# Kernel tuning notes

Hardware: AMD Instinct MI355X
Metric: run time of the kernel (lower is better)

Reference implementation:

```python
import jax, jax.numpy as jnp
import numpy as np

N, C, OUT, E, H = 4096, 256, 256, 131072, 8
DH = C // H
EPS = 1e-5


def layer_norm(h, g, b):
    mu = jnp.mean(h, axis=-1, keepdims=True)
    var = jnp.mean(jnp.square(h - mu), axis=-1, keepdims=True)
    return (h - mu) * jax.lax.rsqrt(var + EPS) * g + b


def setup_inputs() -> dict:
    key = jax.random.key(0)
    ks = jax.random.split(key, 12)
    s = 1.0 / np.sqrt(C)
    return {
        "x": jax.random.normal(ks[0], (N, C), jnp.float32),
        "edge_index": jax.random.randint(ks[1], (2, E), 0, N, jnp.int32),
        "edge_attr": jax.random.normal(ks[2], (E, C), jnp.float32),
        # nn.MultiheadAttention params
        "in_proj_w": jax.random.uniform(ks[3], (3 * C, C), jnp.float32, -s, s),
        "in_proj_b": jnp.zeros((3 * C,), jnp.float32),
        "attn_out_w": jax.random.uniform(ks[4], (C, C), jnp.float32, -s, s),
        "attn_out_b": jnp.zeros((C,), jnp.float32),
        # edge_mlp: Linear(3C -> OUT) + LayerNorm(OUT)
        "edge_w": jax.random.uniform(ks[5], (OUT, 3 * C), jnp.float32, -1 / np.sqrt(3 * C), 1 / np.sqrt(3 * C)),
        "edge_b": jax.random.uniform(ks[6], (OUT,), jnp.float32, -1 / np.sqrt(3 * C), 1 / np.sqrt(3 * C)),
        "ln1_g": jnp.ones((OUT,), jnp.float32),
        "ln1_b": jnp.zeros((OUT,), jnp.float32),
        # output_proj: Linear(C + OUT -> OUT)
        "out_w": jax.random.uniform(ks[7], (OUT, C + OUT), jnp.float32, -1 / np.sqrt(C + OUT), 1 / np.sqrt(C + OUT)),
        "out_b": jax.random.uniform(ks[8], (OUT,), jnp.float32, -1 / np.sqrt(C + OUT), 1 / np.sqrt(C + OUT)),
        "ln2_g": jnp.ones((OUT,), jnp.float32),
        "ln2_b": jnp.zeros((OUT,), jnp.float32),
    }


def reference(x, edge_index, edge_attr, in_proj_w, in_proj_b, attn_out_w, attn_out_b,
              edge_w, edge_b, ln1_g, ln1_b, out_w, out_b, ln2_g, ln2_b):
    num_nodes = x.shape[0]
    # --- dense self-attention over all nodes (seq len = N, batch 1) ---
    qkv = x @ in_proj_w.T + in_proj_b            # [N, 3C]
    q, k, v = jnp.split(qkv, 3, axis=-1)
    q = q.reshape(num_nodes, H, DH).transpose(1, 0, 2)  # [H, N, DH]
    k = k.reshape(num_nodes, H, DH).transpose(1, 0, 2)
    v = v.reshape(num_nodes, H, DH).transpose(1, 0, 2)
    scores = jnp.einsum("hqd,hkd->hqk", q, k) / np.sqrt(DH)
    attn = jax.nn.softmax(scores, axis=-1)       # dropout inactive at eval
    ctx = jnp.einsum("hqk,hkd->hqd", attn, v)    # [H, N, DH]
    ctx = ctx.transpose(1, 0, 2).reshape(num_nodes, C)
    x_attn = ctx @ attn_out_w.T + attn_out_b     # [N, C]
    # --- vectorized edge messages: gather -> MLP -> scatter-add ---
    row, col = edge_index[0], edge_index[1]
    msg_in = jnp.concatenate([x[row], x[col], edge_attr], axis=-1)  # [E, 3C]
    msg = jax.nn.relu(layer_norm(msg_in @ edge_w.T + edge_b, ln1_g, ln1_b))
    node_messages = jax.ops.segment_sum(msg, col, num_segments=num_nodes)  # [N, OUT]
    # --- combine, project, residual, norm ---
    combined = jnp.concatenate([x_attn, node_messages], axis=-1)
    out = combined @ out_w.T + out_b
    out = out + x                                # OUT == C so residual fires
    return layer_norm(out, ln2_g, ln2_b)
```

## Files before the change

kernel.cpp:

```cpp
#include <hip/hip_runtime.h>
#include <hip/hip_bf16.h>
#include <math.h>

typedef __bf16 bf16;
typedef __bf16 bf16x8 __attribute__((ext_vector_type(8)));
typedef __bf16 bf16x4 __attribute__((ext_vector_type(4)));
typedef float f32x4 __attribute__((ext_vector_type(4)));
typedef float f32x16 __attribute__((ext_vector_type(16)));

#define MFMA16(a, b, c) __builtin_amdgcn_mfma_f32_16x16x32_bf16((a), (b), (c), 0, 0, 0)
#define MFMA32(a, b, c) __builtin_amdgcn_mfma_f32_32x32x16_bf16((a), (b), (c), 0, 0, 0)

#define N_NODES 4096
#define C_DIM   256
#define E_EDGES 131072
#define APAD    280
#define TPAD    260

__device__ __forceinline__ float ldf(const void* p, int i, bool f32) {
    return f32 ? ((const float*)p)[i] : (float)((const bf16*)p)[i];
}

__device__ __forceinline__ bf16x8 ld8(const void* base, size_t off, bool f32) {
    if (f32) {
        const float* p = (const float*)base + off;
        float4 a = *(const float4*)p;
        float4 b = *(const float4*)(p + 4);
        bf16x8 r;
        r[0] = (bf16)a.x; r[1] = (bf16)a.y; r[2] = (bf16)a.z; r[3] = (bf16)a.w;
        r[4] = (bf16)b.x; r[5] = (bf16)b.y; r[6] = (bf16)b.z; r[7] = (bf16)b.w;
        return r;
    }
    return *(const bf16x8*)((const bf16*)base + off);
}

__device__ __forceinline__ void ld8f(const void* base, int off, bool f32, float* o) {
    if (f32) {
        float4 a = *(const float4*)((const float*)base + off);
        float4 b = *(const float4*)((const float*)base + off + 4);
        o[0] = a.x; o[1] = a.y; o[2] = a.z; o[3] = a.w;
        o[4] = b.x; o[5] = b.y; o[6] = b.z; o[7] = b.w;
    } else {
        bf16x8 r = *(const bf16x8*)((const bf16*)base + off);
#pragma unroll
        for (int j = 0; j < 8; ++j) o[j] = (float)r[j];
    }
}

__device__ __forceinline__ unsigned cvtpk(float a, float b) {
    unsigned r;
    asm("v_cvt_pk_bf16_f32 %0, %1, %2" : "=v"(r) : "v"(a), "v"(b));
    return r;
}
__device__ __forceinline__ void pl32swap(unsigned &a, unsigned &b) {
    asm volatile("v_permlane32_swap_b32 %0, %1" : "+v"(a), "+v"(b));
}

union PW { unsigned u[4]; bf16x8 v; };

__global__ __launch_bounds__(64) void detect_dtype(const void* x, int* flag)
{
    const bf16* xb = (const bf16*)x;
    int tid = threadIdx.x;
    int bad = 0;
    for (int i = tid; i < 4096; i += 64) {
        float v = fabsf((float)xb[i]);
        if (!(v >= 1e-6f && v <= 100.0f)) bad++;
    }
#pragma unroll
    for (int m = 1; m < 64; m <<= 1) bad += __shfl_xor(bad, m);
    if (tid == 0) *flag = (bad > 400) ? 1 : 0;
}

__global__ __launch_bounds__(256) void convert_inputs(
    const void* s0, const void* s1, const void* s2, const void* s3, const void* s4,
    bf16* dst, const int* flag)
{
    int idx = blockIdx.x * 256 + threadIdx.x;
    const void* src; int local;
    if (idx < 1048576)      { src = s0; local = idx; }
    else if (idx < 1245184) { src = s1; local = idx - 1048576; }
    else if (idx < 1310720) { src = s2; local = idx - 1245184; }
    else if (idx < 1507328) { src = s3; local = idx - 1310720; }
    else                    { src = s4; local = idx - 1507328; }
    if (*flag) dst[idx] = (bf16)(((const float*)src)[local]);
    else ((unsigned short*)dst)[idx] = ((const unsigned short*)src)[local];
}

__global__ __launch_bounds__(256) void edge_hist(
    const int* __restrict__ ecol, int* __restrict__ counts)
{
    int e = blockIdx.x * 256 + threadIdx.x;
    atomicAdd(&counts[ecol[e]], 1);
}

__global__ __launch_bounds__(256) void edge_scan(
    const int* __restrict__ counts, int* __restrict__ offsets,
    int* __restrict__ cursor)
{
    __shared__ int part[256];
    __shared__ int pref[257];
    int t = threadIdx.x;
    int base = t * 16;
    int s = 0;
#pragma unroll
    for (int i = 0; i < 16; ++i) s += counts[base + i];
    part[t] = s;
    __syncthreads();
    if (t == 0) {
        int run = 0;
        for (int i = 0; i < 256; ++i) { pref[i] = run; run += part[i]; }
        pref[256] = run;
    }
    __syncthreads();
    int off = pref[t];
#pragma unroll
    for (int i = 0; i < 16; ++i) {
        offsets[base + i] = off;
        cursor[base + i]  = off;
        off += counts[base + i];
    }
    if (t == 255) offsets[4096] = off;
}

__global__ __launch_bounds__(256) void edge_scatter(
    const int* __restrict__ ecol, int* __restrict__ cursor,
    int* __restrict__ eid)
{
    int e = blockIdx.x * 256 + threadIdx.x;
    int pos = atomicAdd(&cursor[ecol[e]], 1);
    eid[pos] = e;
}

__global__ __launch_bounds__(256) void gemm_bt(
    const bf16* __restrict__ A, int lda,
    const bf16* __restrict__ W, int ldw,
    const void* __restrict__ bias,
    void* __restrict__ Cout, int ldc, int c_f32,
    const bf16* __restrict__ resid, int ldr,
    int K, const int* __restrict__ flag)
{
    const bool f32 = (*flag != 0);
    const int wave = threadIdx.x >> 6;
    const int lane = threadIdx.x & 63;
    const int quad = lane >> 4;
    const int l16  = lane & 15;
    const int m_base = blockIdx.x * 32;
    const int n_base = blockIdx.y * 256 + wave * 64;

    const bf16* a0p = A + (size_t)(m_base + l16) * lda + quad * 8;
    const bf16* a1p = a0p + (size_t)16 * lda;
    const bf16* wp  = W + (size_t)(n_base + l16) * ldw + quad * 8;

    f32x4 acc[2][4] = {};
    for (int k = 0; k < K; k += 32) {
        bf16x8 a0 = *(const bf16x8*)(a0p + k);
        bf16x8 a1 = *(const bf16x8*)(a1p + k);
#pragma unroll
        for (int nt = 0; nt < 4; ++nt) {
            bf16x8 b = *(const bf16x8*)(wp + (size_t)nt * 16 * ldw + k);
            acc[0][nt] = MFMA16(a0, b, acc[0][nt]);
            acc[1][nt] = MFMA16(a1, b, acc[1][nt]);
        }
    }
#pragma unroll
    for (int mt = 0; mt < 2; ++mt) {
#pragma unroll
        for (int nt = 0; nt < 4; ++nt) {
            int col = n_base + nt * 16 + l16;
            float bv = bias ? ldf(bias, col, f32) : 0.0f;
#pragma unroll
            for (int r = 0; r < 4; ++r) {
                int row = m_base + mt * 16 + quad * 4 + r;
                float v = acc[mt][nt][r] + bv;
                if (resid) v += (float)resid[(size_t)row * ldr + col];
                if (c_f32) ((float*)Cout)[(size_t)row * ldc + col] = v;
                else       ((bf16*)Cout)[(size_t)row * ldc + col] = (bf16)v;
            }
        }
    }
}

__global__ __launch_bounds__(256) void transpose_v(
    const bf16* __restrict__ qkv, bf16* __restrict__ vt)
{
    __shared__ bf16 t[32][65];
    const int n0 = blockIdx.x * 64;
    const int c0 = blockIdx.y * 32;
    const int tid = threadIdx.x;
    {
        int cl = tid & 31, nl = tid >> 5;
#pragma unroll
        for (int p = 0; p < 8; ++p) {
            int n = nl + p * 8;
            t[cl][n] = qkv[(size_t)(n0 + n) * 768 + 512 + c0 + cl];
        }
    }
    __syncthreads();
    {
        int nn = tid & 63, cc = tid >> 6;
#pragma unroll
        for (int p = 0; p < 8; ++p) {
            int c = cc + p * 4;
            vt[(size_t)(c0 + c) * 4096 + n0 + nn] = t[c][nn];
        }
    }
}

__global__ __launch_bounds__(256) void attn_kernel(
    const bf16* __restrict__ qkv,
    const bf16* __restrict__ vt,
    bf16* __restrict__ ctx)
{
    __shared__ float oL[4][32][33];
    __shared__ float mS[4][32];
    __shared__ float lS[4][32];
    const int tid  = threadIdx.x;
    const int wave = tid >> 6;
    const int lane = tid & 63;
    const int l32  = lane & 31;
    const int hl   = lane >> 5;
    const int h  = blockIdx.x >> 7;
    const int qt = blockIdx.x & 127;

    const float csc = 1.4426950408889634f * 0.17677669529663687f;

    const bf16* qrow = qkv + (size_t)(qt * 32 + l32) * 768 + h * 32 + hl * 8;
    bf16x8 qf1 = *(const bf16x8*)qrow;
    bf16x8 qf2 = *(const bf16x8*)(qrow + 16);

    const bf16* kbp = qkv + 256 + h * 32 + hl * 8;
    const bf16* vrp = vt + (size_t)(h * 32 + l32) * 4096 + hl * 8;

    float mrun = -INFINITY, msc = -INFINITY, lacc = 0.f;
    f32x16 oacc = {};
    const f32x16 z16 = {};

    const int kbeg = wave * 1024;
    for (int k0 = kbeg; k0 < kbeg + 1024; k0 += 32) {
        const bf16* kp = kbp + (size_t)(k0 + l32) * 768;
        bf16x8 kf1 = *(const bf16x8*)kp;
        bf16x8 kf2 = *(const bf16x8*)(kp + 16);
        bf16x8 vf1 = *(const bf16x8*)(vrp + k0);
        bf16x8 vf2 = *(const bf16x8*)(vrp + k0 + 16);

        f32x16 s = MFMA32(kf1, qf1, z16);
        s = MFMA32(kf2, qf2, s);

        float a0 = fmaxf(fmaxf(s[0], s[1]), fmaxf(s[2], s[3]));
        float a1 = fmaxf(fmaxf(s[4], s[5]), fmaxf(s[6], s[7]));
        float a2 = fmaxf(fmaxf(s[8], s[9]), fmaxf(s[10], s[11]));
        float a3 = fmaxf(fmaxf(s[12], s[13]), fmaxf(s[14], s[15]));
        float tm = fmaxf(fmaxf(a0, a1), fmaxf(a2, a3));
        tm = fmaxf(tm, __shfl_xor(tm, 32));

        if (__any(tm > mrun)) {
            float nm = fmaxf(mrun, tm);
            float nmsc = nm * csc;
            float al = exp2f(msc - nmsc);
            mrun = nm; msc = nmsc;
            lacc *= al;
#pragma unroll
            for (int i = 0; i < 16; ++i) oacc[i] *= al;
        }

        float p[16];
#pragma unroll
        for (int i = 0; i < 16; ++i) {
            p[i] = exp2f(__builtin_fmaf(s[i], csc, -msc));
            lacc += p[i];
        }

        unsigned w0 = cvtpk(p[0], p[1]),  w1 = cvtpk(p[2], p[3]);
        unsigned w2 = cvtpk(p[4], p[5]),  w3 = cvtpk(p[6], p[7]);
        unsigned w4 = cvtpk(p[8], p[9]),  w5 = cvtpk(p[10], p[11]);
        unsigned w6 = cvtpk(p[12], p[13]), w7 = cvtpk(p[14], p[15]);
        pl32swap(w0, w2); pl32swap(w1, w3);
        pl32swap(w4, w6); pl32swap(w5, w7);
        PW f1; f1.u[0] = w0; f1.u[1] = w1; f1.u[2] = w2; f1.u[3] = w3;
        PW f2; f2.u[0] = w4; f2.u[1] = w5; f2.u[2] = w6; f2.u[3] = w7;

        oacc = MFMA32(vf1, f1.v, oacc);
        oacc = MFMA32(vf2, f2.v, oacc);
    }

    lacc += __shfl_xor(lacc, 32);
    if (hl == 0) { mS[wave][l32] = mrun; lS[wave][l32] = lacc; }
#pragma unroll
    for (int i = 0; i < 16; ++i) {
        int d = (i & 3) + 8 * (i >> 2) + 4 * hl;
        oL[wave][l32][d] = oacc[i];
    }
    __syncthreads();
    {
        int q = tid >> 3, d0 = (tid & 7) * 4;
        float m0 = mS[0][q], m1 = mS[1][q], m2 = mS[2][q], m3 = mS[3][q];
        float ms = fmaxf(fmaxf(m0, m1), fmaxf(m2, m3));
        float f0 = exp2f((m0 - ms) * csc), f1 = exp2f((m1 - ms) * csc);
        float f2 = exp2f((m2 - ms) * csc), f3 = exp2f((m3 - ms) * csc);
        float ls = lS[0][q] * f0 + lS[1][q] * f1 + lS[2][q] * f2 + lS[3][q] * f3;
        float inv = 1.0f / ls;
        bf16x4 o4;
#pragma unroll
        for (int i = 0; i < 4; ++i) {
            int d = d0 + i;
            float v = (oL[0][q][d] * f0 + oL[1][q][d] * f1 +
                       oL[2][q][d] * f2 + oL[3][q][d] * f3) * inv;
            o4[i] = (bf16)v;
        }
        *(bf16x4*)(ctx + (size_t)(qt * 32 + q) * 256 + h * 32 + d0) = o4;
    }
}

__global__ __launch_bounds__(256) void edge_msg_v3(
    const int* __restrict__ erow, const int* __restrict__ ecol,
    const void* __restrict__ eattr,
    const bf16* __restrict__ ew,
    const void* __restrict__ eb,
    const void* __restrict__ g1, const void* __restrict__ b1,
    const bf16* __restrict__ U, const bf16* __restrict__ V,
    bf16* __restrict__ msg, const int* __restrict__ flag)
{
    __shared__ char smem[64 * APAD * 2];
    bf16* Asm = (bf16*)smem;
    float (*Trow)[TPAD] = (float(*)[TPAD])smem;

    const bool f32 = (*flag != 0);
    const int tid  = threadIdx.x;
    const int wave = tid >> 6;
    const int lane = tid & 63;
    const int quad = lane >> 4;
    const int l16  = lane & 15;
    const int e_base = blockIdx.x * 64;

    bf16x8 breg[8][4];
#pragma unroll
    for (int k0 = 0; k0 < 8; ++k0)
#pragma unroll
        for (int nt = 0; nt < 4; ++nt)
            breg[k0][nt] = *(const bf16x8*)(ew +
                (size_t)(wave * 64 + nt * 16 + l16) * 768 + 512 + k0 * 32 + quad * 8);

    {
        int row   = tid >> 2;
        int cbase = (tid & 3) * 64;
        bf16* dst = Asm + row * APAD + cbase;
        if (!f32) {
            const bf16* src = (const bf16*)eattr + (size_t)(e_base + row) * 256 + cbase;
#pragma unroll
            for (int j = 0; j < 8; ++j)
                *(bf16x8*)(dst + j * 8) = *(const bf16x8*)(src + j * 8);
        } else {
            const float* src = (const float*)eattr + (size_t)(e_base + row) * 256 + cbase;
#pragma unroll
            for (int j = 0; j < 8; ++j) {
                float4 a = *(const float4*)(src + j * 8);
                float4 b = *(const float4*)(src + j * 8 + 4);
                bf16x8 r;
                r[0] = (bf16)a.x; r[1] = (bf16)a.y; r[2] = (bf16)a.z; r[3] = (bf16)a.w;
                r[4] = (bf16)b.x; r[5] = (bf16)b.y; r[6] = (bf16)b.z; r[7] = (bf16)b.w;
                *(bf16x8*)(dst + j * 8) = r;
            }
        }
    }
    __syncthreads();

    f32x4 acc[4][4] = {};
#pragma unroll
    for (int k0 = 0; k0 < 8; ++k0) {
#pragma unroll
        for (int mt = 0; mt < 4; ++mt) {
            bf16x8 af = *(const bf16x8*)(Asm + (mt * 16 + l16) * APAD + k0 * 32 + quad * 8);
#pragma unroll
            for (int nt = 0; nt < 4; ++nt)
                acc[mt][nt] = MFMA16(af, breg[k0][nt], acc[mt][nt]);
        }
    }

    float ebv[4];
#pragma unroll
    for (int nt = 0; nt < 4; ++nt)
        ebv[nt] = ldf(eb, wave * 64 + nt * 16 + l16, f32);

    for (int p = 0; p < 2; ++p) {
        __syncthreads();
#pragma unroll
        for (int mtl = 0; mtl < 2; ++mtl) {
            int mt = p * 2 + mtl;
#pragma unroll
            for (int nt = 0; nt < 4; ++nt)
#pragma unroll
                for (int r = 0; r < 4; ++r)
                    Trow[mtl * 16 + quad * 4 + r][wave * 64 + nt * 16 + l16] =
                        acc[mt][nt][r] + ebv[nt];
        }
        __syncthreads();
        {
            int row = tid >> 3;
            int seg = tid & 7;
            int e = e_base + p * 32 + row;
            int er = erow[e], ec = ecol[e];
            const float* tr = &Trow[row][seg * 32];
            const bf16* up = U + (size_t)er * 256 + seg * 32;
            const bf16* wp = V + (size_t)ec * 256 + seg * 32;
            float v[32];
            float s = 0.f, q = 0.f;
#pragma unroll
            for (int i = 0; i < 4; ++i) {
                float4 ta = *(const float4*)(tr + i * 8);
                float4 tb = *(const float4*)(tr + i * 8 + 4);
                bf16x8 u8 = *(const bf16x8*)(up + i * 8);
                bf16x8 w8 = *(const bf16x8*)(wp + i * 8);
                float t0 = ta.x + (float)u8[0] + (float)w8[0];
                float t1 = ta.y + (float)u8[1] + (float)w8[1];
                float t2 = ta.z + (float)u8[2] + (float)w8[2];
                float t3 = ta.w + (float)u8[3] + (float)w8[3];
                float t4 = tb.x + (float)u8[4] + (float)w8[4];
                float t5 = tb.y + (float)u8[5] + (float)w8[5];
                float t6 = tb.z + (float)u8[6] + (float)w8[6];
                float t7 = tb.w + (float)u8[7] + (float)w8[7];
                v[i*8+0] = t0; v[i*8+1] = t1; v[i*8+2] = t2; v[i*8+3] = t3;
                v[i*8+4] = t4; v[i*8+5] = t5; v[i*8+6] = t6; v[i*8+7] = t7;
                s += ((t0 + t1) + (t2 + t3)) + ((t4 + t5) + (t6 + t7));
                q = __builtin_fmaf(t0, t0, q); q = __builtin_fmaf(t1, t1, q);
                q = __builtin_fmaf(t2, t2, q); q = __builtin_fmaf(t3, t3, q);
                q = __builtin_fmaf(t4, t4, q); q = __builtin_fmaf(t5, t5, q);
                q = __builtin_fmaf(t6, t6, q); q = __builtin_fmaf(t7, t7, q);
            }
#pragma unroll
            for (int msk = 1; msk < 8; msk <<= 1) {
                s += __shfl_xor(s, msk);
                q += __shfl_xor(q, msk);
            }
            float mean = s * (1.0f / 256.0f);
            float var  = q * (1.0f / 256.0f) - mean * mean;
            float rstd = rsqrtf(var + 1e-5f);
            bf16* op = msg + (size_t)e * 256 + seg * 32;
#pragma unroll
            for (int i = 0; i < 4; ++i) {
                float gv[8], bv[8];
                ld8f(g1, seg * 32 + i * 8, f32, gv);
                ld8f(b1, seg * 32 + i * 8, f32, bv);
                bf16x8 o8;
#pragma unroll
                for (int j = 0; j < 8; ++j)
                    o8[j] = (bf16)fmaxf((v[i*8+j] - mean) * rstd * gv[j] + bv[j], 0.0f);
                *(bf16x8*)(op + i * 8) = o8;
            }
        }
    }
}

__global__ __launch_bounds__(256) void node_gather(
    const bf16* __restrict__ msg,
    const int* __restrict__ offsets, const int* __restrict__ eid,
    bf16* __restrict__ combined)
{
    const int wave = threadIdx.x >> 6, lane = threadIdx.x & 63;
    const int node = blockIdx.x * 4 + wave;
    const int start = offsets[node];
    const int cnt   = offsets[node + 1] - start;
    float a0 = 0.f, a1 = 0.f, a2 = 0.f, a3 = 0.f;
    int i = 0;
    for (; i + 4 <= cnt; i += 4) {
        int e0 = eid[start + i],     e1 = eid[start + i + 1];
        int e2 = eid[start + i + 2], e3 = eid[start + i + 3];
        bf16x4 r0 = *(const bf16x4*)(msg + (size_t)e0 * 256 + lane * 4);
        bf16x4 r1 = *(const bf16x4*)(msg + (size_t)e1 * 256 + lane * 4);
        bf16x4 r2 = *(const bf16x4*)(msg + (size_t)e2 * 256 + lane * 4);
        bf16x4 r3 = *(const bf16x4*)(msg + (size_t)e3 * 256 + lane * 4);
        a0 += (float)r0[0] + (float)r1[0] + (float)r2[0] + (float)r3[0];
        a1 += (float)r0[1] + (float)r1[1] + (float)r2[1] + (float)r3[1];
        a2 += (float)r0[2] + (float)r1[2] + (float)r2[2] + (float)r3[2];
        a3 += (float)r0[3] + (float)r1[3] + (float)r2[3] + (float)r3[3];
    }
    for (; i < cnt; ++i) {
        int e = eid[start + i];
        bf16x4 r = *(const bf16x4*)(msg + (size_t)e * 256 + lane * 4);
        a0 += (float)r[0]; a1 += (float)r[1]; a2 += (float)r[2]; a3 += (float)r[3];
    }
    bf16* cp = combined + (size_t)node * 512 + 256 + lane * 4;
    cp[0] = (bf16)a0; cp[1] = (bf16)a1; cp[2] = (bf16)a2; cp[3] = (bf16)a3;
}

__global__ __launch_bounds__(256) void edge_node(
    const bf16* __restrict__ x,
    const int* __restrict__ erow,
    const void* __restrict__ eattr,
    const bf16* __restrict__ ew,
    const void* __restrict__ eb,
    const void* __restrict__ g1, const void* __restrict__ b1,
    const int* __restrict__ offsets, const int* __restrict__ eid,
    bf16* __restrict__ combined, const int* __restrict__ flag)
{
    __shared__ float part[32][4][2];
    const bool f32 = (*flag != 0);
    const int wave = threadIdx.x >> 6;
    const int lane = threadIdx.x & 63;
    const int quad = lane >> 4;
    const int l16  = lane & 15;
    const int n = blockIdx.x;
    const int start = offsets[n];
    const int cnt   = offsets[n + 1] - start;

    float gv[4], bv[4], ebv[4];
#pragma unroll
    for (int nt = 0; nt < 4; ++nt) {
        int col = wave * 64 + nt * 16 + l16;
        gv[nt]  = ldf(g1, col, f32);
        bv[nt]  = ldf(b1, col, f32);
        ebv[nt] = ldf(eb, col, f32);
    }
    const bf16* wp = ew + (size_t)(wave * 64 + l16) * 768 + quad * 8;
    const bf16* xn = x + (size_t)n * 256 + quad * 8;

    f32x4 acc1[4] = {};
#pragma unroll
    for (int kk = 0; kk < 8; ++kk) {
        bf16x8 a = *(const bf16x8*)(xn + kk * 32);
#pragma unroll
        for (int nt = 0; nt < 4; ++nt) {
            bf16x8 b = *(const bf16x8*)(wp + (size_t)nt * 16 * 768 + 256 + kk * 32);
            acc1[nt] = MFMA16(a, b, acc1[nt]);
        }
    }
    float nacc[4] = {0.f, 0.f, 0.f, 0.f};
    for (int c0 = 0; c0 < cnt; c0 += 32) {
        int i0 = c0 + l16;      i0 = (i0 < cnt) ? i0 : 0;
        int i1 = c0 + 16 + l16; i1 = (i1 < cnt) ? i1 : 0;
        int e0 = eid[start + i0];
        int e1 = eid[start + i1];
        const bf16* xr0 = x + (size_t)erow[e0] * 256 + quad * 8;
        const bf16* xr1 = x + (size_t)erow[e1] * 256 + quad * 8;
        f32x4 acc[2][4];
#pragma unroll
        for (int nt = 0; nt < 4; ++nt) { acc[0][nt] = acc1[nt]; acc[1][nt] = acc1[nt]; }
#pragma unroll
        for (int kk = 0; kk < 8; ++kk) {
            bf16x8 a0 = *(const bf16x8*)(xr0 + kk * 32);
            bf16x8 a1 = *(const bf16x8*)(xr1 + kk * 32);
#pragma unroll
            for (int nt = 0; nt < 4; ++nt) {
                bf16x8 b = *(const bf16x8*)(wp + (size_t)nt * 16 * 768 + kk * 32);
                acc[0][nt] = MFMA16(a0, b, acc[0][nt]);
                acc[1][nt] = MFMA16(a1, b, acc[1][nt]);
            }
        }
#pragma unroll
        for (int kk = 0; kk < 8; ++kk) {
            int koff = quad * 8 + kk * 32;
            bf16x8 a0 = ld8(eattr, (size_t)e0 * 256 + koff, f32);
            bf16x8 a1 = ld8(eattr, (size_t)e1 * 256 + koff, f32);
#pragma unroll
            for (int nt = 0; nt < 4; ++nt) {
                bf16x8 b = *(const bf16x8*)(wp + (size_t)nt * 16 * 768 + 512 + kk * 32);
                acc[0][nt] = MFMA16(a0, b, acc[0][nt]);
                acc[1][nt] = MFMA16(a1, b, acc[1][nt]);
            }
        }
#pragma unroll
        for (int mt = 0; mt < 2; ++mt)
#pragma unroll
            for (int nt = 0; nt < 4; ++nt)
#pragma unroll
                for (int r = 0; r < 4; ++r) acc[mt][nt][r] += ebv[nt];
        float ps[2][4], pq[2][4];
#pragma unroll
        for (int mt = 0; mt < 2; ++mt)
#pragma unroll
            for (int r = 0; r < 4; ++r) {
                float s = 0.f, q = 0.f;
#pragma unroll
                for (int nt = 0; nt < 4; ++nt) {
                    float v = acc[mt][nt][r];
                    s += v; q += v * v;
                }
                ps[mt][r] = s; pq[mt][r] = q;
            }
#pragma unroll
        for (int msk = 1; msk < 16; msk <<= 1)
#pragma unroll
            for (int mt = 0; mt < 2; ++mt)
#pragma unroll
                for (int r = 0; r < 4; ++r) {
                    ps[mt][r] += __shfl_xor(ps[mt][r], msk);
                    pq[mt][r] += __shfl_xor(pq[mt][r], msk);
                }
        if (l16 == 0) {
#pragma unroll
            for (int mt = 0; mt < 2; ++mt)
#pragma unroll
                for (int r = 0; r < 4; ++r) {
                    part[mt * 16 + quad * 4 + r][wave][0] = ps[mt][r];
                    part[mt * 16 + quad * 4 + r][wave][1] = pq[mt][r];
                }
        }
        __syncthreads();
#pragma unroll
        for (int mt = 0; mt < 2; ++mt)
#pragma unroll
            for (int r = 0; r < 4; ++r) {
                int row = mt * 16 + quad * 4 + r;
                float s = part[row][0][0] + part[row][1][0] + part[row][2][0] + part[row][3][0];
                float q = part[row][0][1] + part[row][1][1] + part[row][2][1] + part[row][3][1];
                float mean = s * (1.0f / 256.0f);
                float var  = q * (1.0f / 256.0f) - mean * mean;
                float rstd = rsqrtf(var + 1e-5f);
                if ((c0 + row) < cnt) {
#pragma unroll
                    for (int nt = 0; nt < 4; ++nt) {
                        float val = (acc[mt][nt][r] - mean) * rstd * gv[nt] + bv[nt];
                        nacc[nt] += fmaxf(val, 0.0f);
                    }
                }
            }
        __syncthreads();
    }
#pragma unroll
    for (int nt = 0; nt < 4; ++nt) {
        nacc[nt] += __shfl_xor(nacc[nt], 16);
        nacc[nt] += __shfl_xor(nacc[nt], 32);
    }
    if (quad == 0) {
#pragma unroll
        for (int nt = 0; nt < 4; ++nt)
            combined[(size_t)n * 512 + 256 + wave * 64 + nt * 16 + l16] = (bf16)nacc[nt];
    }
}

__global__ __launch_bounds__(256) void ln_out_kernel(
    const float* __restrict__ pre,
    const void* __restrict__ g, const void* __restrict__ bb,
    void* __restrict__ out, const int* __restrict__ flag)
{
    const bool f32 = (*flag != 0);
    const int wave = threadIdx.x >> 6, lane = threadIdx.x & 63;
    const int row = blockIdx.x * 4 + wave;
    float4 v4 = *(const float4*)(pre + (size_t)row * 256 + lane * 4);
    float v[4] = {v4.x, v4.y, v4.z, v4.w};
    float s  = v[0] + v[1] + v[2] + v[3];
    float sq = v[0]*v[0] + v[1]*v[1] + v[2]*v[2] + v[3]*v[3];
#pragma unroll
    for (int msk = 1; msk < 64; msk <<= 1) {
        s  += __shfl_xor(s, msk);
        sq += __shfl_xor(sq, msk);
    }
    float mean = s * (1.0f / 256.0f);
    float var  = sq * (1.0f / 256.0f) - mean * mean;
    float rstd = rsqrtf(var + 1e-5f);
#pragma unroll
    for (int i = 0; i < 4; ++i) {
        int c = lane * 4 + i;
        float r = (v[i] - mean) * rstd * ldf(g, c, f32) + ldf(bb, c, f32);
        if (f32) ((float*)out)[(size_t)row * 256 + c] = r;
        else     ((bf16*)out)[(size_t)row * 256 + c] = (bf16)r;
    }
}

extern "C" void kernel_launch(void* const* d_in, const int* in_sizes, int n_in,
                              void* d_out, int out_size, void* d_ws, size_t ws_size,
                              hipStream_t stream)
{
    const void* x_raw  = d_in[0];
    const int*  eidx   = (const int*)d_in[1];
    const void* eattr  = d_in[2];
    const void* in_w   = d_in[3];
    const void* in_b   = d_in[4];
    const void* ao_w   = d_in[5];
    const void* ao_b   = d_in[6];
    const void* e_w    = d_in[7];
    const void* e_b    = d_in[8];
    const void* g1     = d_in[9];
    const void* b1     = d_in[10];
    const void* o_w    = d_in[11];
    const void* o_b    = d_in[12];
    const void* g2     = d_in[13];
    const void* b2     = d_in[14];

    char* ws = (char*)d_ws;
    bf16*  qkv      = (bf16*)(ws);
    bf16*  vt       = (bf16*)(ws + 6291456);
    bf16*  ctx      = (bf16*)(ws + 8388608);
    bf16*  combined = (bf16*)(ws + 10485760);
    int*   counts   = (int*)(ws + 14680064);
    int*   offsets  = (int*)(ws + 14696448);
    int*   cursor   = (int*)(ws + 14712848);
    int*   eid      = (int*)(ws + 14729232);
    float* out_pre  = (float*)(ws + 18874368);
    bf16*  U        = (bf16*)(ws + 18874368);
    bf16*  V        = (bf16*)(ws + 20971520);
    bf16*  canon    = (bf16*)(ws + 23068672);
    int*   flag     = (int*)(ws + 26345472);
    bf16*  msg      = (bf16*)(ws + 26345728);

    const size_t WS_NEEDED = 93454592;

    bf16* x_bf   = canon;
    bf16* inw_bf = canon + 1048576;
    bf16* aow_bf = canon + 1245184;
    bf16* ew_bf  = canon + 1310720;
    bf16* ow_bf  = canon + 1507328;

    const int* erow = eidx;
    const int* ecol = eidx + E_EDGES;

    detect_dtype<<<dim3(1), 64, 0, stream>>>(x_raw, flag);
    convert_inputs<<<dim3(6400), 256, 0, stream>>>(x_raw, in_w, ao_w, e_w, o_w,
                                                   canon, flag);
    hipMemsetAsync(counts, 0, 16384, stream);
    edge_hist<<<dim3(E_EDGES / 256), 256, 0, stream>>>(ecol, counts);
    edge_scan<<<dim3(1), 256, 0, stream>>>(counts, offsets, cursor);
    edge_scatter<<<dim3(E_EDGES / 256), 256, 0, stream>>>(ecol, cursor, eid);

    gemm_bt<<<dim3(128, 1), 256, 0, stream>>>(x_bf, 256, ew_bf, 768, nullptr,
                                              U, 256, 0, nullptr, 0, 256, flag);
    gemm_bt<<<dim3(128, 1), 256, 0, stream>>>(x_bf, 256, ew_bf + 256, 768, nullptr,
                                              V, 256, 0, nullptr, 0, 256, flag);

    gemm_bt<<<dim3(128, 3), 256, 0, stream>>>(x_bf, 256, inw_bf, 256, in_b,
                                              qkv, 768, 0, nullptr, 0, 256, flag);
    transpose_v<<<dim3(64, 8), 256, 0, stream>>>(qkv, vt);
    attn_kernel<<<dim3(1024), 256, 0, stream>>>(qkv, vt, ctx);
    gemm_bt<<<dim3(128, 1), 256, 0, stream>>>(ctx, 256, aow_bf, 256, ao_b,
                                              combined, 512, 0, nullptr, 0, 256, flag);
    if (ws_size >= WS_NEEDED) {
        edge_msg_v3<<<dim3(E_EDGES / 64), 256, 0, stream>>>(erow, ecol, eattr,
                                                            ew_bf, e_b, g1, b1,
                                                            U, V, msg, flag);
        node_gather<<<dim3(N_NODES / 4), 256, 0, stream>>>(msg, offsets, eid, combined);
    } else {
        edge_node<<<dim3(N_NODES), 256, 0, stream>>>(x_bf, erow, eattr,
                                                     ew_bf, e_b, g1, b1,
                                                     offsets, eid, combined, flag);
    }
    gemm_bt<<<dim3(128, 1), 256, 0, stream>>>(combined, 512, ow_bf, 512, o_b,
                                              out_pre, 256, 1, x_bf, 256, 512, flag);
    ln_out_kernel<<<dim3(N_NODES / 4), 256, 0, stream>>>(out_pre, g2, b2, d_out, flag);
}
```

Measured before the change: 522.0 us.

## Rewrite edge message kernel register-resident, merge U/V GEMMs, fuse output GEMM with LayerNorm

The edge message kernel now computes the edge_attr projection with A operands loaded straight from global memory into registers, 32 edges per block, and does the bias, U/V gather, LayerNorm and ReLU in the MFMA accumulator layout. Row statistics are reduced with cross-lane shuffles plus a tiny shared array, replacing the large LDS staging and transpose buffers. The two U/V GEMM launches are merged into one grid, and the final projection GEMM is fused with residual add and LayerNorm, removing the fp32 intermediate buffer and one launch. Risks: gathered U/V reads become scalar bf16 loads per element, msg stores are no longer vectorised, and A-tile loads are uncoalesced.

```diff
diff --git a/kernel.cpp b/kernel.cpp
--- a/kernel.cpp
+++ b/kernel.cpp
@@ -14,8 +14,6 @@
 #define N_NODES 4096
 #define C_DIM   256
 #define E_EDGES 131072
-#define APAD    280
-#define TPAD    260
 
 __device__ __forceinline__ float ldf(const void* p, int i, bool f32) {
     return f32 ? ((const float*)p)[i] : (float)((const bf16*)p)[i];
@@ -34,19 +32,6 @@
     return *(const bf16x8*)((const bf16*)base + off);
 }
 
-__device__ __forceinline__ void ld8f(const void* base, int off, bool f32, float* o) {
-    if (f32) {
-        float4 a = *(const float4*)((const float*)base + off);
-        float4 b = *(const float4*)((const float*)base + off + 4);
-        o[0] = a.x; o[1] = a.y; o[2] = a.z; o[3] = a.w;
-        o[4] = b.x; o[5] = b.y; o[6] = b.z; o[7] = b.w;
-    } else {
-        bf16x8 r = *(const bf16x8*)((const bf16*)base + off);
-#pragma unroll
-        for (int j = 0; j < 8; ++j) o[j] = (float)r[j];
-    }
-}
-
 __device__ __forceinline__ unsigned cvtpk(float a, float b) {
     unsigned r;
     asm("v_cvt_pk_bf16_f32 %0, %1, %2" : "=v"(r) : "v"(a), "v"(b));
@@ -179,6 +164,48 @@
             }
         }
     }
+}
+
+__global__ __launch_bounds__(256) void gemm_uv(
+    const bf16* __restrict__ x, const bf16* __restrict__ ew,
+    bf16* __restrict__ U, bf16* __restrict__ V)
+{
+    const int wave = threadIdx.x >> 6;
+    const int lane = threadIdx.x & 63;
+    const int quad = lane >> 4;
+    const int l16  = lane & 15;
+    const int m_base = blockIdx.x * 32;
+    bf16* dst = blockIdx.y ? V : U;
+    const bf16* W = ew + blockIdx.y * 256;
+
+    const bf16* a0p = x + (size_t)(m_base + l16) * 256 + quad * 8;
+    const bf16* a1p = a0p + (size_t)16 * 256;
+    const bf16* wp  = W + (size_t)(wave * 64 + l16) * 768 + quad * 8;
+
+    f32x4 acc[2][4] = {};
+#pragma unroll
+    for (int kk = 0; kk < 8; ++kk) {
+        int k = kk * 32;
+        bf16x8 a0 = *(const bf16x8*)(a0p + k);
+        bf16x8 a1 = *(const bf16x8*)(a1p + k);
+#pragma unroll
+        for (int nt = 0; nt < 4; ++nt) {
+            bf16x8 b = *(const bf16x8*)(wp + (size_t)nt * 16 * 768 + k);
+            acc[0][nt] = MFMA16(a0, b, acc[0][nt]);
+            acc[1][nt] = MFMA16(a1, b, acc[1][nt]);
+        }
+    }
+#pragma unroll
+    for (int mt = 0; mt < 2; ++mt)
+#pragma unroll
+        for (int nt = 0; nt < 4; ++nt) {
+            int col = wave * 64 + nt * 16 + l16;
+#pragma unroll
+            for (int r = 0; r < 4; ++r) {
+                int row = m_base + mt * 16 + quad * 4 + r;
+                dst[(size_t)row * 256 + col] = (bf16)acc[mt][nt][r];
+            }
+        }
 }
 
 __global__ __launch_bounds__(256) void transpose_v(
@@ -312,7 +339,7 @@
     }
 }
 
-__global__ __launch_bounds__(256) void edge_msg_v3(
+__global__ __launch_bounds__(256, 4) void edge_msg_v5(
     const int* __restrict__ erow, const int* __restrict__ ecol,
     const void* __restrict__ eattr,
     const bf16* __restrict__ ew,
@@ -321,134 +348,108 @@
     const bf16* __restrict__ U, const bf16* __restrict__ V,
     bf16* __restrict__ msg, const int* __restrict__ flag)
 {
-    __shared__ char smem[64 * APAD * 2];
-    bf16* Asm = (bf16*)smem;
-    float (*Trow)[TPAD] = (float(*)[TPAD])smem;
-
+    __shared__ float stats[32][4][2];
     const bool f32 = (*flag != 0);
     const int tid  = threadIdx.x;
-    const int wave = tid >> 6;
+    const int colq = tid >> 6;
     const int lane = tid & 63;
     const int quad = lane >> 4;
     const int l16  = lane & 15;
-    const int e_base = blockIdx.x * 64;
-
-    bf16x8 breg[8][4];
-#pragma unroll
-    for (int k0 = 0; k0 < 8; ++k0)
+    const int e_base = blockIdx.x * 32;
+
+    const bf16* wp = ew + (size_t)(colq * 64 + l16) * 768 + 512 + quad * 8;
+
+    f32x4 acc[2][4] = {};
+#pragma unroll
+    for (int k0 = 0; k0 < 8; ++k0) {
+        bf16x8 b[4];
 #pragma unroll
         for (int nt = 0; nt < 4; ++nt)
-            breg[k0][nt] = *(const bf16x8*)(ew +
-                (size_t)(wave * 64 + nt * 16 + l16) * 768 + 512 + k0 * 32 + quad * 8);
-
-    {
-        int row   = tid >> 2;
-        int cbase = (tid & 3) * 64;
-        bf16* dst = Asm + row * APAD + cbase;
-        if (!f32) {
-            const bf16* src = (const bf16*)eattr + (size_t)(e_base + row) * 256 + cbase;
-#pragma unroll
-            for (int j = 0; j < 8; ++j)
-                *(bf16x8*)(dst + j * 8) = *(const bf16x8*)(src + j * 8);
-        } else {
-            const float* src = (const float*)eattr + (size_t)(e_base + row) * 256 + cbase;
-#pragma unroll
-            for (int j = 0; j < 8; ++j) {
-                float4 a = *(const float4*)(src + j * 8);
-                float4 b = *(const float4*)(src + j * 8 + 4);
-                bf16x8 r;
-                r[0] = (bf16)a.x; r[1] = (bf16)a.y; r[2] = (bf16)a.z; r[3] = (bf16)a.w;
-                r[4] = (bf16)b.x; r[5] = (bf16)b.y; r[6] = (bf16)b.z; r[7] = (bf16)b.w;
-                *(bf16x8*)(dst + j * 8) = r;
-            }
-        }
+            b[nt] = *(const bf16x8*)(wp + (size_t)nt * 16 * 768 + k0 * 32);
+#pragma unroll
+        for (int mt = 0; mt < 2; ++mt) {
+            bf16x8 a = ld8(eattr,
+                (size_t)(e_base + mt * 16 + l16) * 256 + k0 * 32 + quad * 8, f32);
+#pragma unroll
+            for (int nt = 0; nt < 4; ++nt)
+                acc[mt][nt] = MFMA16(a, b[nt], acc[mt][nt]);
+        }
+    }
+
+    float ebv[4], glv[4], blv[4];
+#pragma unroll
+    for (int nt = 0; nt < 4; ++nt) {
+        int col = colq * 64 + nt * 16 + l16;
+        ebv[nt] = ldf(eb, col, f32);
+        glv[nt] = ldf(g1, col, f32);
+        blv[nt] = ldf(b1, col, f32);
+    }
+    int erw[2][4], ecl[2][4];
+#pragma unroll
+    for (int mt = 0; mt < 2; ++mt)
+#pragma unroll
+        for (int r = 0; r < 4; ++r) {
+            int e = e_base + mt * 16 + quad * 4 + r;
+            erw[mt][r] = erow[e];
+            ecl[mt][r] = ecol[e];
+        }
+
+    float s[2][4] = {}, q[2][4] = {};
+#pragma unroll
+    for (int mt = 0; mt < 2; ++mt)
+#pragma unroll
+        for (int nt = 0; nt < 4; ++nt) {
+            int col = colq * 64 + nt * 16 + l16;
+#pragma unroll
+            for (int r = 0; r < 4; ++r) {
+                float u = (float)U[(size_t)erw[mt][r] * 256 + col];
+                float v = (float)V[(size_t)ecl[mt][r] * 256 + col];
+                float val = acc[mt][nt][r] + ebv[nt] + u + v;
+                acc[mt][nt][r] = val;
+                s[mt][r] += val;
+                q[mt][r] = __builtin_fmaf(val, val, q[mt][r]);
+            }
+        }
+#pragma unroll
+    for (int msk = 1; msk < 16; msk <<= 1)
+#pragma unroll
+        for (int mt = 0; mt < 2; ++mt)
+#pragma unroll
+            for (int r = 0; r < 4; ++r) {
+                s[mt][r] += __shfl_xor(s[mt][r], msk);
+                q[mt][r] += __shfl_xor(q[mt][r], msk);
+            }
+    if (l16 == 0) {
+#pragma unroll
+        for (int mt = 0; mt < 2; ++mt)
+#pragma unroll
+            for (int r = 0; r < 4; ++r) {
+                int row = mt * 16 + quad * 4 + r;
+                stats[row][colq][0] = s[mt][r];
+                stats[row][colq][1] = q[mt][r];
+            }
     }
     __syncthreads();
-
-    f32x4 acc[4][4] = {};
-#pragma unroll
-    for (int k0 = 0; k0 < 8; ++k0) {
-#pragma unroll
-        for (int mt = 0; mt < 4; ++mt) {
-            bf16x8 af = *(const bf16x8*)(Asm + (mt * 16 + l16) * APAD + k0 * 32 + quad * 8);
-#pragma unroll
-            for (int nt = 0; nt < 4; ++nt)
-                acc[mt][nt] = MFMA16(af, breg[k0][nt], acc[mt][nt]);
-        }
-    }
-
-    float ebv[4];
-#pragma unroll
-    for (int nt = 0; nt < 4; ++nt)
-        ebv[nt] = ldf(eb, wave * 64 + nt * 16 + l16, f32);
-
-    for (int p = 0; p < 2; ++p) {
-        __syncthreads();
-#pragma unroll
-        for (int mtl = 0; mtl < 2; ++mtl) {
-            int mt = p * 2 + mtl;
-#pragma unroll
-            for (int nt = 0; nt < 4; ++nt)
-#pragma unroll
-                for (int r = 0; r < 4; ++r)
-                    Trow[mtl * 16 + quad * 4 + r][wave * 64 + nt * 16 + l16] =
-                        acc[mt][nt][r] + ebv[nt];
-        }
-        __syncthreads();
-        {
-            int row = tid >> 3;
-            int seg = tid & 7;
-            int e = e_base + p * 32 + row;
-            int er = erow[e], ec = ecol[e];
-            const float* tr = &Trow[row][seg * 32];
-            const bf16* up = U + (size_t)er * 256 + seg * 32;
-            const bf16* wp = V + (size_t)ec * 256 + seg * 32;
-            float v[32];
-            float s = 0.f, q = 0.f;
-#pragma unroll
-            for (int i = 0; i < 4; ++i) {
-                float4 ta = *(const float4*)(tr + i * 8);
-                float4 tb = *(const float4*)(tr + i * 8 + 4);
-                bf16x8 u8 = *(const bf16x8*)(up + i * 8);
-                bf16x8 w8 = *(const bf16x8*)(wp + i * 8);
-                float t0 = ta.x + (float)u8[0] + (float)w8[0];
-                float t1 = ta.y + (float)u8[1] + (float)w8[1];
-                float t2 = ta.z + (float)u8[2] + (float)w8[2];
-                float t3 = ta.w + (float)u8[3] + (float)w8[3];
-                float t4 = tb.x + (float)u8[4] + (float)w8[4];
-                float t5 = tb.y + (float)u8[5] + (float)w8[5];
-                float t6 = tb.z + (float)u8[6] + (float)w8[6];
-                float t7 = tb.w + (float)u8[7] + (float)w8[7];
-                v[i*8+0] = t0; v[i*8+1] = t1; v[i*8+2] = t2; v[i*8+3] = t3;
-                v[i*8+4] = t4; v[i*8+5] = t5; v[i*8+6] = t6; v[i*8+7] = t7;
-                s += ((t0 + t1) + (t2 + t3)) + ((t4 + t5) + (t6 + t7));
-                q = __builtin_fmaf(t0, t0, q); q = __builtin_fmaf(t1, t1, q);
-                q = __builtin_fmaf(t2, t2, q); q = __builtin_fmaf(t3, t3, q);
-                q = __builtin_fmaf(t4, t4, q); q = __builtin_fmaf(t5, t5, q);
-                q = __builtin_fmaf(t6, t6, q); q = __builtin_fmaf(t7, t7, q);
-            }
-#pragma unroll
-            for (int msk = 1; msk < 8; msk <<= 1) {
-                s += __shfl_xor(s, msk);
-                q += __shfl_xor(q, msk);
-            }
-            float mean = s * (1.0f / 256.0f);
-            float var  = q * (1.0f / 256.0f) - mean * mean;
+#pragma unroll
+    for (int mt = 0; mt < 2; ++mt)
+#pragma unroll
+        for (int r = 0; r < 4; ++r) {
+            int row = mt * 16 + quad * 4 + r;
+            float ss = (stats[row][0][0] + stats[row][1][0]) +
+                       (stats[row][2][0] + stats[row][3][0]);
+            float qq = (stats[row][0][1] + stats[row][1][1]) +
+                       (stats[row][2][1] + stats[row][3][1]);
+            float mean = ss * (1.0f / 256.0f);
+            float var  = qq * (1.0f / 256.0f) - mean * mean;
             float rstd = rsqrtf(var + 1e-5f);
-            bf16* op = msg + (size_t)e * 256 + seg * 32;
-#pragma unroll
-            for (int i = 0; i < 4; ++i) {
-                float gv[8], bv[8];
-                ld8f(g1, seg * 32 + i * 8, f32, gv);
-                ld8f(b1, seg * 32 + i * 8, f32, bv);
-                bf16x8 o8;
-#pragma unroll
-                for (int j = 0; j < 8; ++j)
-                    o8[j] = (bf16)fmaxf((v[i*8+j] - mean) * rstd * gv[j] + bv[j], 0.0f);
-                *(bf16x8*)(op + i * 8) = o8;
-            }
-        }
-    }
+            bf16* op = msg + (size_t)(e_base + row) * 256;
+#pragma unroll
+            for (int nt = 0; nt < 4; ++nt) {
+                int col = colq * 64 + nt * 16 + l16;
+                float o = fmaxf((acc[mt][nt][r] - mean) * rstd * glv[nt] + blv[nt], 0.0f);
+                op[col] = (bf16)o;
+            }
+        }
 }
 
 __global__ __launch_bounds__(256) void node_gather(
@@ -628,32 +629,83 @@
     }
 }
 
-__global__ __launch_bounds__(256) void ln_out_kernel(
-    const float* __restrict__ pre,
+__global__ __launch_bounds__(256) void gemm_ln(
+    const bf16* __restrict__ A,
+    const bf16* __restrict__ W,
+    const void* __restrict__ bias,
+    const bf16* __restrict__ resid,
     const void* __restrict__ g, const void* __restrict__ bb,
     void* __restrict__ out, const int* __restrict__ flag)
 {
+    __shared__ float stats[16][4][2];
     const bool f32 = (*flag != 0);
-    const int wave = threadIdx.x >> 6, lane = threadIdx.x & 63;
-    const int row = blockIdx.x * 4 + wave;
-    float4 v4 = *(const float4*)(pre + (size_t)row * 256 + lane * 4);
-    float v[4] = {v4.x, v4.y, v4.z, v4.w};
-    float s  = v[0] + v[1] + v[2] + v[3];
-    float sq = v[0]*v[0] + v[1]*v[1] + v[2]*v[2] + v[3]*v[3];
-#pragma unroll
-    for (int msk = 1; msk < 64; msk <<= 1) {
-        s  += __shfl_xor(s, msk);
-        sq += __shfl_xor(sq, msk);
-    }
-    float mean = s * (1.0f / 256.0f);
-    float var  = sq * (1.0f / 256.0f) - mean * mean;
-    float rstd = rsqrtf(var + 1e-5f);
-#pragma unroll
-    for (int i = 0; i < 4; ++i) {
-        int c = lane * 4 + i;
-        float r = (v[i] - mean) * rstd * ldf(g, c, f32) + ldf(bb, c, f32);
-        if (f32) ((float*)out)[(size_t)row * 256 + c] = r;
-        else     ((bf16*)out)[(size_t)row * 256 + c] = (bf16)r;
+    const int wave = threadIdx.x >> 6;
+    const int lane = threadIdx.x & 63;
+    const int quad = lane >> 4;
+    const int l16  = lane & 15;
+    const int m_base = blockIdx.x * 16;
+
+    const bf16* ap = A + (size_t)(m_base + l16) * 512 + quad * 8;
+    const bf16* wp = W + (size_t)(wave * 64 + l16) * 512 + quad * 8;
+
+    f32x4 acc[4] = {};
+#pragma unroll
+    for (int kk = 0; kk < 16; ++kk) {
+        int k = kk * 32;
+        bf16x8 a = *(const bf16x8*)(ap + k);
+#pragma unroll
+        for (int nt = 0; nt < 4; ++nt) {
+            bf16x8 b = *(const bf16x8*)(wp + (size_t)nt * 16 * 512 + k);
+            acc[nt] = MFMA16(a, b, acc[nt]);
+        }
+    }
+    float s[4] = {}, q[4] = {};
+#pragma unroll
+    for (int nt = 0; nt < 4; ++nt) {
+        int col = wave * 64 + nt * 16 + l16;
+        float bv = ldf(bias, col, f32);
+#pragma unroll
+        for (int r = 0; r < 4; ++r) {
+            int row = m_base + quad * 4 + r;
+            float v = acc[nt][r] + bv + (float)resid[(size_t)row * 256 + col];
+            acc[nt][r] = v;
+            s[r] += v;
+            q[r] = __builtin_fmaf(v, v, q[r]);
+        }
+    }
+#pragma unroll
+    for (int msk = 1; msk < 16; msk <<= 1)
+#pragma unroll
+        for (int r = 0; r < 4; ++r) {
+            s[r] += __shfl_xor(s[r], msk);
+            q[r] += __shfl_xor(q[r], msk);
+        }
+    if (l16 == 0) {
+#pragma unroll
+        for (int r = 0; r < 4; ++r) {
+            stats[quad * 4 + r][wave][0] = s[r];
+            stats[quad * 4 + r][wave][1] = q[r];
+        }
+    }
+    __syncthreads();
+#pragma unroll
+    for (int r = 0; r < 4; ++r) {
+        int row16 = quad * 4 + r;
+        float ss = (stats[row16][0][0] + stats[row16][1][0]) +
+                   (stats[row16][2][0] + stats[row16][3][0]);
+        float qq = (stats[row16][0][1] + stats[row16][1][1]) +
+                   (stats[row16][2][1] + stats[row16][3][1]);
+        float mean = ss * (1.0f / 256.0f);
+        float var  = qq * (1.0f / 256.0f) - mean * mean;
+        float rstd = rsqrtf(var + 1e-5f);
+        int row = m_base + row16;
+#pragma unroll
+        for (int nt = 0; nt < 4; ++nt) {
+            int col = wave * 64 + nt * 16 + l16;
+            float o = (acc[nt][r] - mean) * rstd * ldf(g, col, f32) + ldf(bb, col, f32);
+            if (f32) ((float*)out)[(size_t)row * 256 + col] = o;
+            else     ((bf16*)out)[(size_t)row * 256 + col] = (bf16)o;
+        }
     }
 }
 
@@ -686,7 +738,6 @@
     int*   offsets  = (int*)(ws + 14696448);
     int*   cursor   = (int*)(ws + 14712848);
     int*   eid      = (int*)(ws + 14729232);
-    float* out_pre  = (float*)(ws + 18874368);
     bf16*  U        = (bf16*)(ws + 18874368);
     bf16*  V        = (bf16*)(ws + 20971520);
     bf16*  canon    = (bf16*)(ws + 23068672);
@@ -712,10 +763,7 @@
     edge_scan<<<dim3(1), 256, 0, stream>>>(counts, offsets, cursor);
     edge_scatter<<<dim3(E_EDGES / 256), 256, 0, stream>>>(ecol, cursor, eid);
 
-    gemm_bt<<<dim3(128, 1), 256, 0, stream>>>(x_bf, 256, ew_bf, 768, nullptr,
-                                              U, 256, 0, nullptr, 0, 256, flag);
-    gemm_bt<<<dim3(128, 1), 256, 0, stream>>>(x_bf, 256, ew_bf + 256, 768, nullptr,
-                                              V, 256, 0, nullptr, 0, 256, flag);
+    gemm_uv<<<dim3(128, 2), 256, 0, stream>>>(x_bf, ew_bf, U, V);
 
     gemm_bt<<<dim3(128, 3), 256, 0, stream>>>(x_bf, 256, inw_bf, 256, in_b,
                                               qkv, 768, 0, nullptr, 0, 256, flag);
@@ -724,7 +772,7 @@
     gemm_bt<<<dim3(128, 1), 256, 0, stream>>>(ctx, 256, aow_bf, 256, ao_b,
                                               combined, 512, 0, nullptr, 0, 256, flag);
     if (ws_size >= WS_NEEDED) {
-        edge_msg_v3<<<dim3(E_EDGES / 64), 256, 0, stream>>>(erow, ecol, eattr,
+        edge_msg_v5<<<dim3(E_EDGES / 32), 256, 0, stream>>>(erow, ecol, eattr,
                                                             ew_bf, e_b, g1, b1,
                                                             U, V, msg, flag);
         node_gather<<<dim3(N_NODES / 4), 256, 0, stream>>>(msg, offsets, eid, combined);
@@ -733,7 +781,6 @@
                                                      ew_bf, e_b, g1, b1,
                                                      offsets, eid, combined, flag);
     }
-    gemm_bt<<<dim3(128, 1), 256, 0, stream>>>(combined, 512, ow_bf, 512, o_b,
-                                              out_pre, 256, 1, x_bf, 256, 512, flag);
-    ln_out_kernel<<<dim3(N_NODES / 4), 256, 0, stream>>>(out_pre, g2, b2, d_out, flag);
-}
+    gemm_ln<<<dim3(256), 256, 0, stream>>>(combined, ow_bf, o_b, x_bf,
+                                           g2, b2, d_out, flag);
+}
```

After: 517.4 us. About the same (-0.9%).
